# Optimization experiments

Hardware: AMD Instinct MI355X
Metric: run time of the kernel (lower is better)

The kernel has to match this reference:

```python
import jax, jax.numpy as jnp
import numpy as np

DEPTH = 6
N_LEAVES = 2 ** DEPTH


def setup_inputs() -> dict:
    key = jax.random.key(0)
    ks = jax.random.split(key, 7)
    in_f, lw, out_f = 1024, 64, 512
    B = 4096
    s1 = 1.0 / np.sqrt(in_f)
    s2 = 1.0 / np.sqrt(lw)
    return {
        "x": jax.random.normal(ks[0], (B, in_f), jnp.float32),
        "node_weights": jax.random.uniform(ks[1], (N_LEAVES - 1, in_f), jnp.float32, -s1, s1),
        "node_biases": jax.random.uniform(ks[2], (N_LEAVES - 1, 1), jnp.float32, -s1, s1),
        "w1s": jax.random.uniform(ks[3], (N_LEAVES, in_f, lw), jnp.float32, -s1, s1),
        "b1s": jax.random.uniform(ks[4], (N_LEAVES, lw), jnp.float32, -s1, s1),
        "w2s": jax.random.uniform(ks[5], (N_LEAVES, lw, out_f), jnp.float32, -s2, s2),
        "b2s": jax.random.uniform(ks[6], (N_LEAVES, out_f), jnp.float32, -s2, s2),
    }


def _fff_forward(x, node_weights, node_biases, w1s, b1s, w2s, b2s):
    B = x.shape[0]
    # Soft routing: build per-leaf mixture weights level by level (training path).
    mixture = jnp.ones((B, N_LEAVES), x.dtype)
    for d in range(DEPTH):
        platform = 2 ** d - 1
        n_nodes = 2 ** d
        w = node_weights[platform:platform + n_nodes]          # (n, in)
        b = node_biases[platform:platform + n_nodes]            # (n, 1)
        logits = x @ w.T + b.T                                  # (B, n)
        be = jax.nn.sigmoid(logits)
        mod = jnp.stack([1.0 - be, be], axis=-1).reshape(B, 2 * n_nodes)
        mixture = (mixture.reshape(B, 2 * n_nodes, N_LEAVES // (2 * n_nodes))
                   * mod[:, :, None]).reshape(B, N_LEAVES)
    # All-leaf expert MLPs (grouped GEMMs), then mixture-weighted sum.
    h = jax.nn.relu(jnp.einsum('bi,liw->blw', x, w1s) + b1s[None])   # (B, L, W)
    y = jnp.einsum('blw,lwo->blo', h, w2s) + b2s[None]                # (B, L, O)
    return jnp.sum(y * mixture[:, :, None], axis=1)                   # (B, O)


def reference(x, node_weights, node_biases, w1s, b1s, w2s, b2s):
    return _fff_forward(x, node_weights, node_biases, w1s, b1s, w2s, b2s)
```

## Files before the change

kernel.cpp:

```cpp
#include <hip/hip_runtime.h>
#include <hip/hip_bf16.h>

typedef unsigned short u16;
typedef __attribute__((ext_vector_type(8))) short bf16x8;
typedef __attribute__((ext_vector_type(4))) float f32x4;
typedef __attribute__((ext_vector_type(16))) float f32x16;
typedef __attribute__((ext_vector_type(4))) unsigned short u16x4;
typedef __attribute__((ext_vector_type(8))) unsigned short u16x8;

#define BATCH 4096
#define INF   1024
#define NH    4096
#define OUTF  512
#define NLEAF 64
#define FDEPTH 6
#define ZSPL  4

__device__ __align__(16) u16  g_Xb[(size_t)BATCH * INF];
__device__ __align__(16) u16  g_W1t[(size_t)NH * INF];
__device__ __align__(16) u16  g_W2t[(size_t)OUTF * NH];
__device__ __align__(16) u16  g_NWh[(size_t)64 * INF];
__device__ __align__(16) u16  g_B2t[(size_t)OUTF * 64];
__device__ __align__(16) u16  g_Hb[(size_t)BATCH * NH];
__device__ __align__(16) float g_mix[(size_t)BATCH * NLEAF];
__device__ __align__(16) float g_part[(size_t)ZSPL * BATCH * OUTF];

__device__ inline u16 f2b(float f) {
  __hip_bfloat16 h = __float2bfloat16(f);
  return *reinterpret_cast<u16*>(&h);
}

__device__ inline void async16(const u16* g, u16* l) {
  __builtin_amdgcn_global_load_lds((const __attribute__((address_space(1))) void*)g,
                                   (__attribute__((address_space(3))) void*)l, 16, 0, 0);
}

__global__ __launch_bounds__(256) void prep_kernel(
    const float* __restrict__ x, const float* __restrict__ nw,
    const float* __restrict__ w1s, const float* __restrict__ w2s,
    const float* __restrict__ b2s) {
  __shared__ float tile[64 * 65];
  const int b = blockIdx.x;
  const int t = threadIdx.x;

  if (b < 2048) {
    int i = (b * 256 + t) * 8;
    float4 v0 = *(const float4*)(x + i);
    float4 v1 = *(const float4*)(x + i + 4);
    u16x8 h;
    h[0] = f2b(v0.x); h[1] = f2b(v0.y); h[2] = f2b(v0.z); h[3] = f2b(v0.w);
    h[4] = f2b(v1.x); h[5] = f2b(v1.y); h[6] = f2b(v1.z); h[7] = f2b(v1.w);
    *(u16x8*)(g_Xb + i) = h;
    return;
  }
  if (b < 2112) {
    int idx = ((b - 2048) * 256 + t) * 4;
    int n = idx >> 10;
    float4 v = make_float4(0.f, 0.f, 0.f, 0.f);
    if (n < 63) v = *(const float4*)(nw + idx);
    u16x4 h;
    h[0] = f2b(v.x); h[1] = f2b(v.y); h[2] = f2b(v.z); h[3] = f2b(v.w);
    *(u16x4*)(g_NWh + idx) = h;
    return;
  }

  const float* sb;
  u16* db;
  int R, C, r0, c0;
  if (b < 3136) {
    int idx = b - 2112;
    int z = idx >> 4;
    R = 1024; C = 64;
    r0 = (idx & 15) * 64; c0 = 0;
    sb = w1s + (size_t)z * R * C;
    db = g_W1t + (size_t)z * R * C;
  } else if (b < 3648) {
    int idx = b - 3136;
    R = 4096; C = 512;
    r0 = (idx >> 3) * 64; c0 = (idx & 7) * 64;
    sb = w2s;
    db = g_W2t;
  } else {
    int idx = b - 3648;
    R = 64; C = 512;
    r0 = 0; c0 = idx * 64;
    sb = b2s;
    db = g_B2t;
  }
  int cc4 = (t & 15) * 4;
#pragma unroll
  for (int it = 0; it < 4; ++it) {
    int rr = (t >> 4) + it * 16;
    float4 v = *(const float4*)(sb + (size_t)(r0 + rr) * C + c0 + cc4);
    tile[rr * 65 + cc4 + 0] = v.x;
    tile[rr * 65 + cc4 + 1] = v.y;
    tile[rr * 65 + cc4 + 2] = v.z;
    tile[rr * 65 + cc4 + 3] = v.w;
  }
  __syncthreads();
  int cc = t >> 2, rch = (t & 3) * 16;
  u16x8 o0, o1;
#pragma unroll
  for (int j = 0; j < 8; ++j) o0[j] = f2b(tile[(rch + j) * 65 + cc]);
#pragma unroll
  for (int j = 0; j < 8; ++j) o1[j] = f2b(tile[(rch + 8 + j) * 65 + cc]);
  u16* p = db + (size_t)(c0 + cc) * R + r0 + rch;
  *(u16x8*)p = o0;
  *(u16x8*)(p + 8) = o1;
}

__global__ __launch_bounds__(256) void mixture_kernel(
    const float* __restrict__ nb, float* __restrict__ out) {
  __shared__ __align__(16) unsigned char lds[57344];
  const int t = threadIdx.x;
  const int wv = t >> 6, ln = t & 63;
  const int quad = ln >> 4, m16 = ln & 15;
  const int r0 = blockIdx.x * 16;

  u16* stW = (u16*)(lds + wv * 10240);
  u16* stX = (u16*)(lds + wv * 10240 + 8192);
  float* lred = (float*)lds;
  float* ssig = (float*)(lds + 16384);
  u16* smixb = (u16*)(lds + 20480);
  u16* b2l = (u16*)(lds + 24576);

  f32x4 acc[4] = {};
#pragma unroll 1
  for (int it = 0; it < 4; ++it) {
    int kc = wv * 256 + it * 64;
#pragma unroll
    for (int j = 0; j < 8; ++j) {
      int id = j * 64 + ln;
      int row = id >> 3, c8 = (id & 7) ^ (row & 7);
      async16(g_NWh + (size_t)row * INF + kc + c8 * 8, stW + j * 512);
    }
#pragma unroll
    for (int j = 0; j < 2; ++j) {
      int id = j * 64 + ln;
      int row = id >> 3, c8 = (id & 7) ^ (row & 7);
      async16(g_Xb + (size_t)(r0 + row) * INF + kc + c8 * 8, stX + j * 512);
    }
    __syncthreads();
#pragma unroll
    for (int ks = 0; ks < 2; ++ks) {
      bf16x8 bF = *(const bf16x8*)(stX + m16 * 64 + ((ks * 4 + quad) ^ (m16 & 7)) * 8);
#pragma unroll
      for (int tw = 0; tw < 4; ++tw) {
        int row = tw * 16 + m16;
        bf16x8 aF = *(const bf16x8*)(stW + row * 64 + ((ks * 4 + quad) ^ (row & 7)) * 8);
        acc[tw] = __builtin_amdgcn_mfma_f32_16x16x32_bf16(aF, bF, acc[tw], 0, 0, 0);
      }
    }
    __syncthreads();
  }
#pragma unroll
  for (int tw = 0; tw < 4; ++tw)
#pragma unroll
    for (int r = 0; r < 4; ++r)
      lred[((size_t)wv * 64 + tw * 16 + quad * 4 + r) * 16 + m16] = acc[tw][r];
  __syncthreads();

#pragma unroll
  for (int j = 0; j < 8; ++j) {
    int id = (wv * 8 + j) * 64 + ln;
    int row = id >> 3, c8 = (id & 7) ^ (row & 7);
    async16(g_B2t + (size_t)row * 64 + c8 * 8, b2l + (wv * 8 + j) * 512);
  }

  {
    int n = t & 63, rg = t >> 6;
#pragma unroll
    for (int rr = 0; rr < 4; ++rr) {
      int row = rg * 4 + rr;
      float s = lred[(0 * 64 + n) * 16 + row] + lred[(1 * 64 + n) * 16 + row] +
                lred[(2 * 64 + n) * 16 + row] + lred[(3 * 64 + n) * 16 + row];
      if (n < 63) s += nb[n];
      ssig[row * 64 + n] = 1.f / (1.f + __expf(-s));
    }
  }
  __syncthreads();
  {
    int leaf = t & 63, rg = t >> 6;
#pragma unroll
    for (int rr = 0; rr < 4; ++rr) {
      int row = rg * 4 + rr;
      float p = 1.f;
#pragma unroll
      for (int d = 0; d < FDEPTH; ++d) {
        int node = (1 << d) - 1 + (leaf >> (FDEPTH - d));
        int bit = (leaf >> (FDEPTH - 1 - d)) & 1;
        float s = ssig[row * 64 + node];
        p *= bit ? s : (1.f - s);
      }
      g_mix[(size_t)(r0 + row) * 64 + leaf] = p;
      smixb[row * 64 + ((leaf >> 3) ^ (row & 7)) * 8 + (leaf & 7)] = f2b(p);
    }
  }
  __syncthreads();

  bf16x8 mixF[2];
#pragma unroll
  for (int ks = 0; ks < 2; ++ks)
    mixF[ks] = *(const bf16x8*)(smixb + m16 * 64 + ((ks * 4 + quad) ^ (m16 & 7)) * 8);
#pragma unroll 1
  for (int s = 0; s < 2; ++s) {
    f32x4 sacc[4] = {};
#pragma unroll
    for (int tile = 0; tile < 4; ++tile) {
#pragma unroll
      for (int ks = 0; ks < 2; ++ks) {
        int lrow = wv * 64 + tile * 16 + m16;
        bf16x8 aF = *(const bf16x8*)(b2l + lrow * 64 + ((ks * 4 + quad) ^ (lrow & 7)) * 8);
        sacc[tile] = __builtin_amdgcn_mfma_f32_16x16x32_bf16(aF, mixF[ks], sacc[tile], 0, 0, 0);
      }
    }
#pragma unroll
    for (int tile = 0; tile < 4; ++tile) {
      int o = s * 256 + wv * 64 + tile * 16 + quad * 4;
      *(f32x4*)(out + (size_t)(r0 + m16) * OUTF + o) = sacc[tile];
    }
    if (s == 0) {
      __syncthreads();
#pragma unroll
      for (int j = 0; j < 8; ++j) {
        int id = (wv * 8 + j) * 64 + ln;
        int row = id >> 3, c8 = (id & 7) ^ (row & 7);
        async16(g_B2t + (size_t)(256 + row) * 64 + c8 * 8, b2l + (wv * 8 + j) * 512);
      }
      __syncthreads();
    }
  }
}

__global__ __launch_bounds__(256) void gemm1_kernel(const float* __restrict__ b1) {
  constexpr int BM = 128, BN = 128, BK = 64, K = 1024, LD = 1024;

  __shared__ u16 lsA[BM * BK];
  __shared__ u16 lsB[BN * BK];

  const int t = threadIdx.x;
  const int wv = t >> 6, ln = t & 63;
  const int wm = wv >> 1, wn = wv & 1;
  const int l32 = ln & 31, lh = ln >> 5;
  const int am0 = blockIdx.y * BM;
  const int bn0 = blockIdx.x * BN;

  f32x16 acc[2][2] = {};

  for (int kc = 0; kc < K; kc += BK) {
#pragma unroll
    for (int i = 0; i < 4; ++i) {
      int id = i * 256 + t;
      int row = id >> 3;
      int c8 = (id & 7) ^ (row & 7);
      async16(g_Xb + (size_t)(am0 + row) * LD + kc + c8 * 8, lsA + (i * 256 + wv * 64) * 8);
    }
#pragma unroll
    for (int i = 0; i < 4; ++i) {
      int id = i * 256 + t;
      int row = id >> 3;
      int c8 = (id & 7) ^ (row & 7);
      async16(g_W1t + (size_t)(bn0 + row) * LD + kc + c8 * 8, lsB + (i * 256 + wv * 64) * 8);
    }
    __syncthreads();
#pragma unroll
    for (int ks = 0; ks < 4; ++ks) {
      bf16x8 wF[2], xF[2];
#pragma unroll
      for (int tw = 0; tw < 2; ++tw) {
        int row = wn * 64 + tw * 32 + l32;
        wF[tw] = *(const bf16x8*)(lsB + row * BK + ((ks * 2 + lh) ^ (row & 7)) * 8);
      }
#pragma unroll
      for (int tb = 0; tb < 2; ++tb) {
        int row = wm * 64 + tb * 32 + l32;
        xF[tb] = *(const bf16x8*)(lsA + row * BK + ((ks * 2 + lh) ^ (row & 7)) * 8);
      }
#pragma unroll
      for (int tw = 0; tw < 2; ++tw)
#pragma unroll
        for (int tb = 0; tb < 2; ++tb)
          acc[tw][tb] = __builtin_amdgcn_mfma_f32_32x32x16_bf16(wF[tw], xF[tb], acc[tw][tb], 0, 0, 0);
    }
    __syncthreads();
  }

  const int leaf = (bn0 >> 6) + wn;
#pragma unroll
  for (int tb = 0; tb < 2; ++tb) {
    int bg = am0 + wm * 64 + tb * 32 + l32;
    float mixv = g_mix[(size_t)bg * 64 + leaf];
#pragma unroll
    for (int tw = 0; tw < 2; ++tw) {
#pragma unroll
      for (int g = 0; g < 4; ++g) {
        int col0 = bn0 + wn * 64 + tw * 32 + g * 8 + lh * 4;
        float4 b1v = *(const float4*)(b1 + col0);
        u16x4 pk;
        pk[0] = f2b(fmaxf(acc[tw][tb][g * 4 + 0] + b1v.x, 0.f) * mixv);
        pk[1] = f2b(fmaxf(acc[tw][tb][g * 4 + 1] + b1v.y, 0.f) * mixv);
        pk[2] = f2b(fmaxf(acc[tw][tb][g * 4 + 2] + b1v.z, 0.f) * mixv);
        pk[3] = f2b(fmaxf(acc[tw][tb][g * 4 + 3] + b1v.w, 0.f) * mixv);
        *(u16x4*)(g_Hb + (size_t)bg * NH + col0) = pk;
      }
    }
  }
}

__global__ __launch_bounds__(256) void gemm2_kernel() {
  constexpr int BM = 128, BN = 128, BK = 64, K = 4096, LD = 4096;

  __shared__ u16 lsA[BM * BK];
  __shared__ u16 lsB[BN * BK];

  const int bid = blockIdx.x;
  const int xcd = bid & 7, slot = bid >> 3;
  const int ytile = xcd * 4 + (slot >> 4);
  const int rem = slot & 15;
  const int xtile = rem & 3, zidx = rem >> 2;

  const int t = threadIdx.x;
  const int wv = t >> 6, ln = t & 63;
  const int wm = wv >> 1, wn = wv & 1;
  const int quad = ln >> 4, m16 = ln & 15;
  const int am0 = ytile * BM;
  const int bn0 = xtile * BN;
  const int kbeg = zidx * (K / ZSPL);
  const int kend = kbeg + K / ZSPL;

  f32x4 acc[4][4] = {};

  for (int kc = kbeg; kc < kend; kc += BK) {
#pragma unroll
    for (int i = 0; i < 4; ++i) {
      int id = i * 256 + t;
      int row = id >> 3;
      int c8 = (id & 7) ^ (row & 7);
      async16(g_Hb + (size_t)(am0 + row) * LD + kc + c8 * 8, lsA + (i * 256 + wv * 64) * 8);
    }
#pragma unroll
    for (int i = 0; i < 4; ++i) {
      int id = i * 256 + t;
      int row = id >> 3;
      int c8 = (id & 7) ^ (row & 7);
      async16(g_W2t + (size_t)(bn0 + row) * LD + kc + c8 * 8, lsB + (i * 256 + wv * 64) * 8);
    }
    __syncthreads();
#pragma unroll
    for (int ks = 0; ks < 2; ++ks) {
      bf16x8 wF[4], xF[4];
#pragma unroll
      for (int tw = 0; tw < 4; ++tw) {
        int row = wn * 64 + tw * 16 + m16;
        wF[tw] = *(const bf16x8*)(lsB + row * BK + ((ks * 4 + quad) ^ (row & 7)) * 8);
      }
#pragma unroll
      for (int tb = 0; tb < 4; ++tb) {
        int row = wm * 64 + tb * 16 + m16;
        xF[tb] = *(const bf16x8*)(lsA + row * BK + ((ks * 4 + quad) ^ (row & 7)) * 8);
      }
#pragma unroll
      for (int tw = 0; tw < 4; ++tw)
#pragma unroll
        for (int tb = 0; tb < 4; ++tb)
          acc[tw][tb] = __builtin_amdgcn_mfma_f32_16x16x32_bf16(wF[tw], xF[tb], acc[tw][tb], 0, 0, 0);
    }
    __syncthreads();
  }

  float* part = g_part + (size_t)zidx * ((size_t)BATCH * OUTF);
#pragma unroll
  for (int tw = 0; tw < 4; ++tw) {
    int og = bn0 + wn * 64 + tw * 16 + quad * 4;
#pragma unroll
    for (int tb = 0; tb < 4; ++tb) {
      int bg = am0 + wm * 64 + tb * 16 + m16;
      *(f32x4*)(part + (size_t)bg * OUTF + og) = acc[tw][tb];
    }
  }
}

__global__ __launch_bounds__(256) void reduce_kernel(float* __restrict__ out) {
  int i = (blockIdx.x * 256 + threadIdx.x) * 4;
  float4 s = *(const float4*)(out + i);
#pragma unroll
  for (int z = 0; z < ZSPL; ++z) {
    const float4 p = *(const float4*)(g_part + (size_t)z * BATCH * OUTF + i);
    s.x += p.x; s.y += p.y; s.z += p.z; s.w += p.w;
  }
  *(float4*)(out + i) = s;
}

extern "C" void kernel_launch(void* const* d_in, const int* in_sizes, int n_in,
                              void* d_out, int out_size, void* d_ws, size_t ws_size,
                              hipStream_t stream) {
  const float* x = (const float*)d_in[0];
  const float* nw = (const float*)d_in[1];
  const float* nb = (const float*)d_in[2];
  const float* w1s = (const float*)d_in[3];
  const float* b1s = (const float*)d_in[4];
  const float* w2s = (const float*)d_in[5];
  const float* b2s = (const float*)d_in[6];
  float* out = (float*)d_out;
  (void)d_ws; (void)ws_size;

  hipLaunchKernelGGL(prep_kernel, dim3(3656), dim3(256), 0, stream,
                     x, nw, w1s, w2s, b2s);
  hipLaunchKernelGGL(mixture_kernel, dim3(256), dim3(256), 0, stream, nb, out);
  hipLaunchKernelGGL(gemm1_kernel, dim3(32, 32), dim3(256), 0, stream, b1s);
  hipLaunchKernelGGL(gemm2_kernel, dim3(512), dim3(256), 0, stream);
  hipLaunchKernelGGL(reduce_kernel, dim3(2048), dim3(256), 0, stream, out);
}
```

Before: 200.8 us.

## Rewrite gemm1 as 256x256 tile with 4-stage async LDS pipeline

```diff
diff --git a/kernel.cpp b/kernel.cpp
--- a/kernel.cpp
+++ b/kernel.cpp
@@ -232,77 +232,124 @@
   }
 }
 
-__global__ __launch_bounds__(256) void gemm1_kernel(const float* __restrict__ b1) {
-  constexpr int BM = 128, BN = 128, BK = 64, K = 1024, LD = 1024;
-
-  __shared__ u16 lsA[BM * BK];
-  __shared__ u16 lsB[BN * BK];
+__global__ __launch_bounds__(512, 2) void gemm1_kernel(const float* __restrict__ b1) {
+  __shared__ __align__(16) u16 s_lds[65536];
+  u16* lsA = s_lds;
+  u16* lsB = s_lds + 32768;
 
   const int t = threadIdx.x;
   const int wv = t >> 6, ln = t & 63;
-  const int wm = wv >> 1, wn = wv & 1;
-  const int l32 = ln & 31, lh = ln >> 5;
-  const int am0 = blockIdx.y * BM;
-  const int bn0 = blockIdx.x * BN;
-
-  f32x16 acc[2][2] = {};
-
-  for (int kc = 0; kc < K; kc += BK) {
-#pragma unroll
-    for (int i = 0; i < 4; ++i) {
-      int id = i * 256 + t;
-      int row = id >> 3;
-      int c8 = (id & 7) ^ (row & 7);
-      async16(g_Xb + (size_t)(am0 + row) * LD + kc + c8 * 8, lsA + (i * 256 + wv * 64) * 8);
-    }
-#pragma unroll
-    for (int i = 0; i < 4; ++i) {
-      int id = i * 256 + t;
-      int row = id >> 3;
-      int c8 = (id & 7) ^ (row & 7);
-      async16(g_W1t + (size_t)(bn0 + row) * LD + kc + c8 * 8, lsB + (i * 256 + wv * 64) * 8);
-    }
-    __syncthreads();
-#pragma unroll
-    for (int ks = 0; ks < 4; ++ks) {
-      bf16x8 wF[2], xF[2];
-#pragma unroll
-      for (int tw = 0; tw < 2; ++tw) {
-        int row = wn * 64 + tw * 32 + l32;
-        wF[tw] = *(const bf16x8*)(lsB + row * BK + ((ks * 2 + lh) ^ (row & 7)) * 8);
-      }
-#pragma unroll
-      for (int tb = 0; tb < 2; ++tb) {
-        int row = wm * 64 + tb * 32 + l32;
-        xF[tb] = *(const bf16x8*)(lsA + row * BK + ((ks * 2 + lh) ^ (row & 7)) * 8);
-      }
-#pragma unroll
-      for (int tw = 0; tw < 2; ++tw)
-#pragma unroll
-        for (int tb = 0; tb < 2; ++tb)
-          acc[tw][tb] = __builtin_amdgcn_mfma_f32_32x32x16_bf16(wF[tw], xF[tb], acc[tw][tb], 0, 0, 0);
-    }
-    __syncthreads();
-  }
-
-  const int leaf = (bn0 >> 6) + wn;
-#pragma unroll
-  for (int tb = 0; tb < 2; ++tb) {
-    int bg = am0 + wm * 64 + tb * 32 + l32;
-    float mixv = g_mix[(size_t)bg * 64 + leaf];
-#pragma unroll
-    for (int tw = 0; tw < 2; ++tw) {
-#pragma unroll
-      for (int g = 0; g < 4; ++g) {
-        int col0 = bn0 + wn * 64 + tw * 32 + g * 8 + lh * 4;
-        float4 b1v = *(const float4*)(b1 + col0);
-        u16x4 pk;
-        pk[0] = f2b(fmaxf(acc[tw][tb][g * 4 + 0] + b1v.x, 0.f) * mixv);
-        pk[1] = f2b(fmaxf(acc[tw][tb][g * 4 + 1] + b1v.y, 0.f) * mixv);
-        pk[2] = f2b(fmaxf(acc[tw][tb][g * 4 + 2] + b1v.z, 0.f) * mixv);
-        pk[3] = f2b(fmaxf(acc[tw][tb][g * 4 + 3] + b1v.w, 0.f) * mixv);
-        *(u16x4*)(g_Hb + (size_t)bg * NH + col0) = pk;
-      }
+  const int quad = ln >> 4, m16 = ln & 15;
+  const int wm = wv >> 2, wn = wv & 3;
+  const int M0 = (blockIdx.x & 15) * 256;
+  const int N0 = (blockIdx.x >> 4) * 256;
+
+  const int rhalf = ln >> 2;
+  const int qg = (ln & 3) ^ (rhalf & 3);
+  const u16* pA = g_W1t + (size_t)(M0 + wv * 32 + rhalf) * 1024 + qg * 8;
+  const u16* pB = g_Xb + (size_t)(N0 + wv * 32 + rhalf) * 1024 + qg * 8;
+  const int dst0 = wv * 1024;
+
+  const int qx = (quad ^ (m16 & 3)) * 8;
+  const int aro = (wm * 128 + m16) * 32 + qx;
+  const int bro = (wn * 64 + m16) * 32 + qx;
+
+  f32x4 acc[8][4] = {};
+  bf16x8 bF[4];
+
+#define STAGE_A(SLOT, TCOL)                                \
+  do {                                                     \
+    const u16* gs = pA + (TCOL);                           \
+    u16* dd = lsA + (SLOT) * 8192 + dst0;                  \
+    async16(gs, dd);                                       \
+    async16(gs + 16 * 1024, dd + 512);                     \
+  } while (0)
+#define STAGE_B(SLOT, TCOL)                                \
+  do {                                                     \
+    const u16* gs = pB + (TCOL);                           \
+    u16* dd = lsB + (SLOT) * 8192 + dst0;                  \
+    async16(gs, dd);                                       \
+    async16(gs + 16 * 1024, dd + 512);                     \
+  } while (0)
+
+#define G1_PHASE(ASLOT, BSLOT, AH, RELOAD_B, STAGE_STMT, VMCNT_STMT)        \
+  {                                                                         \
+    const u16* Abase = lsA + (ASLOT) * 8192;                                \
+    bf16x8 aF[4];                                                           \
+    _Pragma("unroll") for (int f = 0; f < 4; ++f)                           \
+        aF[f] = *(const bf16x8*)(Abase + aro + ((AH) * 4 + f) * 512);       \
+    if (RELOAD_B) {                                                         \
+      const u16* Bbase = lsB + (BSLOT) * 8192;                              \
+      _Pragma("unroll") for (int f = 0; f < 4; ++f)                         \
+          bF[f] = *(const bf16x8*)(Bbase + bro + f * 512);                  \
+    }                                                                       \
+    STAGE_STMT;                                                             \
+    __builtin_amdgcn_s_barrier();                                           \
+    asm volatile("s_waitcnt lgkmcnt(0)" ::: "memory");                      \
+    __builtin_amdgcn_sched_barrier(0);                                      \
+    __builtin_amdgcn_s_setprio(1);                                          \
+    _Pragma("unroll") for (int f = 0; f < 4; ++f)                           \
+        _Pragma("unroll") for (int g = 0; g < 4; ++g)                       \
+            acc[(AH) * 4 + f][g] = __builtin_amdgcn_mfma_f32_16x16x32_bf16( \
+                aF[f], bF[g], acc[(AH) * 4 + f][g], 0, 0, 0);               \
+    __builtin_amdgcn_s_setprio(0);                                          \
+    VMCNT_STMT;                                                             \
+    __builtin_amdgcn_s_barrier();                                           \
+  }
+
+  STAGE_B(0, 0);
+  STAGE_A(0, 0);
+  STAGE_B(1, 32);
+  STAGE_A(1, 32);
+  STAGE_B(2, 64);
+  STAGE_A(2, 64);
+  STAGE_B(3, 96);
+  asm volatile("s_waitcnt vmcnt(6)" ::: "memory");
+  __builtin_amdgcn_s_barrier();
+
+#pragma unroll 1
+  for (int i = 0; i < 8; ++i) {
+    const int c1 = (2 * i + 1) * 64;
+    const int c2 = ((2 * i + 2) & 15) * 64;
+    const int c3 = ((2 * i + 3) & 15) * 64;
+    G1_PHASE(0, 0, 0, 1, STAGE_A(3, c1 + 32), (void)0);
+    G1_PHASE(0, 0, 1, 0, STAGE_B(0, c2), (void)0);
+    G1_PHASE(1, 1, 0, 1, STAGE_A(0, c2), (void)0);
+    G1_PHASE(1, 1, 1, 0, STAGE_B(1, c2 + 32),
+             asm volatile("s_waitcnt vmcnt(6)" ::: "memory"));
+    G1_PHASE(2, 2, 0, 1, STAGE_A(1, c2 + 32), (void)0);
+    G1_PHASE(2, 2, 1, 0, STAGE_B(2, c3), (void)0);
+    G1_PHASE(3, 3, 0, 1, STAGE_A(2, c3), (void)0);
+    G1_PHASE(3, 3, 1, 0, STAGE_B(3, c3 + 32),
+             asm volatile("s_waitcnt vmcnt(6)" ::: "memory"));
+  }
+#undef G1_PHASE
+#undef STAGE_A
+#undef STAGE_B
+
+  asm volatile("s_waitcnt vmcnt(0)" ::: "memory");
+
+  const int lb = (M0 >> 6) + wm * 2;
+  float2 mx[4];
+#pragma unroll
+  for (int fb = 0; fb < 4; ++fb) {
+    int bb = N0 + wn * 64 + fb * 16 + m16;
+    mx[fb] = *(const float2*)(g_mix + (size_t)bb * 64 + lb);
+  }
+#pragma unroll
+  for (int fa = 0; fa < 8; ++fa) {
+    int n0 = M0 + wm * 128 + fa * 16 + quad * 4;
+    float4 b1v = *(const float4*)(b1 + n0);
+#pragma unroll
+    for (int fb = 0; fb < 4; ++fb) {
+      int bb = N0 + wn * 64 + fb * 16 + m16;
+      float mixv = (fa < 4) ? mx[fb].x : mx[fb].y;
+      u16x4 pk;
+      pk[0] = f2b(fmaxf(acc[fa][fb][0] + b1v.x, 0.f) * mixv);
+      pk[1] = f2b(fmaxf(acc[fa][fb][1] + b1v.y, 0.f) * mixv);
+      pk[2] = f2b(fmaxf(acc[fa][fb][2] + b1v.z, 0.f) * mixv);
+      pk[3] = f2b(fmaxf(acc[fa][fb][3] + b1v.w, 0.f) * mixv);
+      *(u16x4*)(g_Hb + (size_t)bb * NH + n0) = pk;
     }
   }
 }
@@ -407,7 +454,7 @@
   hipLaunchKernelGGL(prep_kernel, dim3(3656), dim3(256), 0, stream,
                      x, nw, w1s, w2s, b2s);
   hipLaunchKernelGGL(mixture_kernel, dim3(256), dim3(256), 0, stream, nb, out);
-  hipLaunchKernelGGL(gemm1_kernel, dim3(32, 32), dim3(256), 0, stream, b1s);
+  hipLaunchKernelGGL(gemm1_kernel, dim3(256), dim3(512), 0, stream, b1s);
   hipLaunchKernelGGL(gemm2_kernel, dim3(512), dim3(256), 0, stream);
   hipLaunchKernelGGL(reduce_kernel, dim3(2048), dim3(256), 0, stream, out);
 }
```

After: 191.5 us. 4.6% less time.
